# Kernel optimization log

Hardware: AMD Instinct MI355X
Metric: run time of the kernel (lower is better)

The kernel has to match this reference:

```python
import jax, jax.numpy as jnp
import numpy as np

ALPHA_MIN = float(np.exp(-1.0 / 5.0))   # 0.8187
ALPHA_MAX = float(np.exp(-1.0 / 25.0))  # 0.9608
THRESHOLD = 1.0


def setup_inputs() -> dict:
    key = jax.random.key(0)
    k_x, k_w, k_a, k_u, k_s = jax.random.split(key, 5)
    B, T, I, H = 64, 1000, 1024, 1024
    x = jax.random.normal(k_x, (B, T, I), dtype=jnp.float32)
    # nn.Linear default init ~ U(-1/sqrt(I), 1/sqrt(I)); gaussian of similar scale is fine
    W = jax.random.normal(k_w, (H, I), dtype=jnp.float32) / np.sqrt(I)
    alpha = jax.random.uniform(k_a, (H,), dtype=jnp.float32,
                               minval=ALPHA_MIN, maxval=ALPHA_MAX)
    # original uses torch.rand for initial membrane potential / spikes
    u0 = jax.random.uniform(k_u, (B, H), dtype=jnp.float32)
    s0 = jax.random.uniform(k_s, (B, H), dtype=jnp.float32)
    return {"x": x, "W": W, "alpha": alpha, "u0": u0, "s0": s0}


def reference(x, W, alpha, u0, s0):
    # Input projection: Wx[b,t,h] = sum_i x[b,t,i] * W[h,i]
    Wx = jnp.einsum('bti,hi->bth', x, W)
    a = jnp.clip(alpha, ALPHA_MIN, ALPHA_MAX)  # [H]

    def step(carry, wx_t):
        ut, st = carry                              # each [B, H]
        ut = a * (ut - st) + (1.0 - a) * wx_t       # leaky integrate with reset
        st = (ut - THRESHOLD > 0).astype(ut.dtype)  # hard spike (boxcar surrogate in bwd)
        return (ut, st), st

    # scan over time: Wx -> [T, B, H]
    _, s = jax.lax.scan(step, (u0, s0), jnp.swapaxes(Wx, 0, 1))
    return jnp.swapaxes(s, 0, 1)  # [B, T, H]
```

## Files before the change

kernel.cpp:

```cpp
#include <hip/hip_runtime.h>


#define TM 128
#define TN 64
#define TK 8
#define LDA 130

__global__ __launch_bounds__(256) void transpose_w(
    const float* __restrict__ W, double* __restrict__ WdT)
{
    __shared__ float t[32][33];
    const int k0 = blockIdx.x * 32;
    const int n0 = blockIdx.y * 32;
    const int tx = threadIdx.x & 31;
    const int ty = threadIdx.x >> 5;
    #pragma unroll
    for (int i = 0; i < 4; i++)
        t[ty + 8 * i][tx] = W[(size_t)(n0 + ty + 8 * i) * 1024 + k0 + tx];
    __syncthreads();
    #pragma unroll
    for (int i = 0; i < 4; i++)
        WdT[(size_t)(k0 + ty + 8 * i) * 1024 + n0 + tx] = (double)t[tx][ty + 8 * i];
}

__global__ __launch_bounds__(256, 3) void gemm_f64_sgpr(
    const float* __restrict__ A,
    const double* __restrict__ WdT,
    double* __restrict__ C, int M, int N, int K)
{
    __shared__ double As[2][TK][LDA];

    const int tid  = threadIdx.x;
    const int lane = tid & 63;
    const int nb = __builtin_amdgcn_readfirstlane(blockIdx.x * TN + (tid >> 6) * 16);
    const int tm = blockIdx.y * TM;

    const int kq = (tid & 1) * 4;
    const int r  = tid >> 1;

    double acc0[16], acc1[16];
    #pragma unroll
    for (int j = 0; j < 16; j++) { acc0[j] = 0.0; acc1[j] = 0.0; }

    const int ar = min(tm + r, M - 1);
    const float* Ap = A + (size_t)ar * K + kq;

    {
        const float4 a0 = *(const float4*)(Ap);
        As[0][kq + 0][r] = (double)a0.x; As[0][kq + 1][r] = (double)a0.y;
        As[0][kq + 2][r] = (double)a0.z; As[0][kq + 3][r] = (double)a0.w;
    }
    __syncthreads();

    auto compute_tile = [&](int p, int k0) {
        #pragma unroll
        for (int kk = 0; kk < TK; kk++) {
            const double* wr = WdT + (size_t)(k0 + kk) * N + nb;
            const double2 a = *(const double2*)&As[p][kk][2 * lane];
            #pragma unroll
            for (int j = 0; j < 16; j++) {
                const double wj = wr[j];
                acc0[j] = fma(a.x, wj, acc0[j]);
                acc1[j] = fma(a.y, wj, acc1[j]);
            }
        }
    };

    const int NS = K / TK;
    for (int s = 0; s < NS - 1; ++s) {
        const int p = s & 1;
        {
            const float4 a0 = *(const float4*)(Ap + (size_t)(s + 1) * TK);
            const int q = 1 - p;
            As[q][kq + 0][r] = (double)a0.x; As[q][kq + 1][r] = (double)a0.y;
            As[q][kq + 2][r] = (double)a0.z; As[q][kq + 3][r] = (double)a0.w;
        }
        compute_tile(p, s * TK);
        __syncthreads();
    }
    compute_tile((NS - 1) & 1, (NS - 1) * TK);

    const int m0 = tm + 2 * lane;
    if (m0 < M) {
        double* Cr = C + (size_t)m0 * N + nb;
        #pragma unroll
        for (int j = 0; j < 8; j++)
            *(double2*)&Cr[2 * j] = double2{acc0[2 * j], acc0[2 * j + 1]};
    }
    if (m0 + 1 < M) {
        double* Cr = C + (size_t)(m0 + 1) * N + nb;
        #pragma unroll
        for (int j = 0; j < 8; j++)
            *(double2*)&Cr[2 * j] = double2{acc1[2 * j], acc1[2 * j + 1]};
    }
}

__global__ __launch_bounds__(256) void lif_scan_kernel(
    const double* __restrict__ Wx,
    const float* __restrict__ alpha,
    const float* __restrict__ u0,
    const float* __restrict__ s0,
    float* __restrict__ out,
    int b0, int T, int H)
{
    const int idx = blockIdx.x * blockDim.x + threadIdx.x;
    const int h  = idx & 1023;
    const int bl = idx >> 10;
    const int b  = b0 + bl;

    const double AMIN = 0.8187307530779818;
    const double AMAX = 0.9607894391523232;
    double a = (double)alpha[h];
    a = fmin(fmax(a, AMIN), AMAX);
    const double oma = 1.0 - a;

    double u = (double)u0[(size_t)b * H + h];
    double s = (double)s0[(size_t)b * H + h];

    const double* wp = Wx + (size_t)bl * T * H + h;
    float* op = out + (size_t)b * T * H + h;

    double v[8];
    #pragma unroll
    for (int p = 0; p < 8; p++) v[p] = wp[(size_t)p * H];

    for (int t0 = 0; t0 < T; t0 += 8) {
        double nv[8];
        const bool more = (t0 + 8) < T;
        const double* wn = wp + (size_t)(t0 + 8) * H;
        #pragma unroll
        for (int p = 0; p < 8; p++) nv[p] = more ? wn[(size_t)p * H] : 0.0;

        #pragma unroll
        for (int p = 0; p < 8; p++) {
            u = a * (u - s) + oma * v[p];
            s = (u - 1.0 > 0.0) ? 1.0 : 0.0;
            op[(size_t)(t0 + p) * H] = (float)s;
        }
        #pragma unroll
        for (int p = 0; p < 8; p++) v[p] = nv[p];
    }
}

extern "C" void kernel_launch(void* const* d_in, const int* in_sizes, int n_in,
                              void* d_out, int out_size, void* d_ws, size_t ws_size,
                              hipStream_t stream) {
    const float* x     = (const float*)d_in[0];
    const float* W     = (const float*)d_in[1];
    const float* alpha = (const float*)d_in[2];
    const float* u0    = (const float*)d_in[3];
    const float* s0    = (const float*)d_in[4];
    float* out = (float*)d_out;
    const int Bt = 64, T = 1000, I = 1024, H = 1024;

    double* wdT = (double*)d_ws;
    const size_t wdT_bytes = (size_t)I * H * sizeof(double);
    double* wx = (double*)((char*)d_ws + wdT_bytes);
    const size_t avail = (ws_size > wdT_bytes) ? ws_size - wdT_bytes : 0;

    const size_t per_batch = (size_t)T * H * sizeof(double);
    int Bc = 1;
    {
        const int cands[7] = {64, 32, 16, 8, 4, 2, 1};
        for (int c = 0; c < 7; c++) {
            if ((size_t)cands[c] * per_batch <= avail) { Bc = cands[c]; break; }
        }
    }

    transpose_w<<<dim3(1024 / 32, 1024 / 32), 256, 0, stream>>>(W, wdT);

    for (int b0 = 0; b0 < Bt; b0 += Bc) {
        const int M = Bc * T;
        dim3 grid(H / TN, (M + TM - 1) / TM);
        gemm_f64_sgpr<<<grid, 256, 0, stream>>>(
            x + (size_t)b0 * T * I, wdT, wx, M, H, I);
        lif_scan_kernel<<<(Bc * H) / 256, 256, 0, stream>>>(
            wx, alpha, u0, s0, out, b0, T, H);
    }
}
```

Before: 2.989 ms.

## Use FP64 MFMA matrix cores for input projection GEMM with runtime layout probe

Adds an FP64 GEMM built on the 16x16x4 f64 MFMA instruction, with both A and W tiles staged in shared memory and double-buffered. A one-wavefront probe kernel works out the MFMA operand and result layout at runtime and stores it in a flag. The MFMA kernel reads that flag and the old scalar FMA kernel serves as a fallback, so both are launched every batch chunk and one exits early. The goal is to move the dominant FP64 GEMM off the vector ALUs onto the matrix cores, at the cost of an extra kernel launch per chunk and a small probe kernel.

After: 2.438 ms. 1.23x faster.

```diff
diff --git a/kernel.cpp b/kernel.cpp
--- a/kernel.cpp
+++ b/kernel.cpp
@@ -3,8 +3,12 @@
 
 #define TM 128
 #define TN 64
-#define TK 8
+#define MTK 16
+#define VTK 8
 #define LDA 130
+#define LDB 66
+
+typedef double v4d __attribute__((ext_vector_type(4)));
 
 __global__ __launch_bounds__(256) void transpose_w(
     const float* __restrict__ W, double* __restrict__ WdT)
@@ -23,12 +27,180 @@
         WdT[(size_t)(k0 + ty + 8 * i) * 1024 + n0 + tx] = (double)t[tx][ty + 8 * i];
 }
 
+__global__ __launch_bounds__(64) void probe_mfma_layout(unsigned int* __restrict__ flag)
+{
+    __shared__ double Am[16][4];
+    __shared__ double Bm[4][16];
+    const int l = threadIdx.x;
+    Am[l & 15][l >> 4] = (double)(1 + (l & 15) + 16 * (l >> 4));
+    Bm[l >> 4][l & 15] = 1.0 + 0.5 * (double)((l >> 4) + 4 * (l & 15));
+    __syncthreads();
+    const v4d z = {0.0, 0.0, 0.0, 0.0};
+    const double a0 = Am[l & 15][l >> 4];
+    const double b0 = Bm[l >> 4][l & 15];
+    const double a1 = Am[l >> 2][l & 3];
+    const double b1 = Bm[l & 3][l >> 2];
+    const v4d d0 = __builtin_amdgcn_mfma_f64_16x16x4f64(a0, b0, z, 0, 0, 0);
+    const v4d d1 = __builtin_amdgcn_mfma_f64_16x16x4f64(a1, b1, z, 0, 0, 0);
+    int ok[8];
+    #pragma unroll
+    for (int c = 0; c < 8; c++) ok[c] = 1;
+    #pragma unroll
+    for (int q = 0; q < 4; q++) {
+        const int iD[4] = {4 * (l >> 4) + q, l & 15, (l >> 4) + 4 * q, l & 15};
+        const int jD[4] = {l & 15, 4 * (l >> 4) + q, l & 15, (l >> 4) + 4 * q};
+        #pragma unroll
+        for (int dm = 0; dm < 4; dm++) {
+            double ref = 0.0;
+            #pragma unroll
+            for (int k = 0; k < 4; k++) ref += Am[iD[dm]][k] * Bm[k][jD[dm]];
+            if (d0[q] != ref) ok[dm] = 0;
+            if (d1[q] != ref) ok[4 + dm] = 0;
+        }
+    }
+    unsigned int f = 255u;
+    for (int c = 7; c >= 0; --c)
+        if (__all(ok[c])) f = (unsigned int)c;
+    if (l == 0) *flag = f;
+}
+
+__global__ __launch_bounds__(256, 3) void gemm_f64_mfma(
+    const float* __restrict__ A,
+    const double* __restrict__ WdT,
+    double* __restrict__ C, int M, int N, int K,
+    const unsigned int* __restrict__ flag)
+{
+    const unsigned int f = *flag;
+    if (f - 1u > 6u) return;
+
+    __shared__ double As[2][MTK][LDA];
+    __shared__ double Bs[2][MTK][LDB];
+
+    const int tid  = threadIdx.x;
+    const int lane = tid & 63;
+    const int l16  = lane & 15;
+    const int kq4  = lane >> 4;
+    const int wid  = tid >> 6;
+    const int wr   = wid >> 1;
+    const int wc   = wid & 1;
+
+    const int imap = (int)(f >> 2);
+    const int dmap = (int)(f & 3u);
+    const int rowl = imap ? (lane >> 2) : l16;
+    const int kl   = imap ? (lane & 3)  : kq4;
+    int rloc, rstep, cloc, cstep;
+    switch (dmap) {
+        case 0:  rloc = 4 * kq4; rstep = 1; cloc = l16;     cstep = 0; break;
+        case 1:  rloc = l16;     rstep = 0; cloc = 4 * kq4; cstep = 1; break;
+        case 2:  rloc = kq4;     rstep = 4; cloc = l16;     cstep = 0; break;
+        default: rloc = l16;     rstep = 0; cloc = kq4;     cstep = 4; break;
+    }
+
+    const int nb0 = blockIdx.x * TN;
+    const int tm  = blockIdx.y * TM;
+
+    const int rA  = tid >> 1;
+    const int kA  = (tid & 1) * 4;
+    const int kkB = tid >> 4;
+    const int cBl = (tid & 15) * 4;
+
+    v4d acc[4][2];
+    #pragma unroll
+    for (int i = 0; i < 4; i++)
+        #pragma unroll
+        for (int j = 0; j < 2; j++)
+            acc[i][j] = (v4d)0.0;
+
+    const int ar = min(tm + rA, M - 1);
+    const float* Apg = A + (size_t)ar * K;
+    const double* Bpg = WdT + (size_t)kkB * N + nb0 + cBl;
+
+    struct StReg { float4 a0, a1; double2 b0, b1; };
+    auto issue = [&](int s) {
+        StReg t;
+        const int k0 = s * MTK;
+        t.a0 = *(const float4*)(Apg + k0 + kA);
+        t.a1 = *(const float4*)(Apg + k0 + kA + 8);
+        const double* wp = Bpg + (size_t)k0 * N;
+        t.b0 = *(const double2*)(wp);
+        t.b1 = *(const double2*)(wp + 2);
+        return t;
+    };
+    auto commit = [&](int buf, const StReg& t) {
+        As[buf][kA + 0][rA] = (double)t.a0.x;
+        As[buf][kA + 1][rA] = (double)t.a0.y;
+        As[buf][kA + 2][rA] = (double)t.a0.z;
+        As[buf][kA + 3][rA] = (double)t.a0.w;
+        As[buf][kA + 8][rA] = (double)t.a1.x;
+        As[buf][kA + 9][rA] = (double)t.a1.y;
+        As[buf][kA + 10][rA] = (double)t.a1.z;
+        As[buf][kA + 11][rA] = (double)t.a1.w;
+        Bs[buf][kkB][cBl + 0] = t.b0.x;
+        Bs[buf][kkB][cBl + 1] = t.b0.y;
+        Bs[buf][kkB][cBl + 2] = t.b1.x;
+        Bs[buf][kkB][cBl + 3] = t.b1.y;
+    };
+
+    const int mw = wr * 64;
+    const int nw = wc * 32;
+    auto compute_tile = [&](int p) {
+        #pragma unroll
+        for (int ks = 0; ks < 4; ++ks) {
+            const int kk = ks * 4 + kl;
+            double av[4], bv[2];
+            #pragma unroll
+            for (int i = 0; i < 4; i++) av[i] = As[p][kk][mw + i * 16 + rowl];
+            #pragma unroll
+            for (int j = 0; j < 2; j++) bv[j] = Bs[p][kk][nw + j * 16 + rowl];
+            #pragma unroll
+            for (int i = 0; i < 4; i++)
+                #pragma unroll
+                for (int j = 0; j < 2; j++)
+                    acc[i][j] = __builtin_amdgcn_mfma_f64_16x16x4f64(
+                        av[i], bv[j], acc[i][j], 0, 0, 0);
+        }
+    };
+
+    commit(0, issue(0));
+    __syncthreads();
+
+    const int NR = K / MTK;
+    for (int s = 0; s < NR - 1; ++s) {
+        const int p = s & 1;
+        StReg t = issue(s + 1);
+        compute_tile(p);
+        commit(1 - p, t);
+        __syncthreads();
+    }
+    compute_tile((NR - 1) & 1);
+
+    const int mwR = tm + mw;
+    const int nwC = nb0 + nw;
+    #pragma unroll
+    for (int i = 0; i < 4; i++) {
+        #pragma unroll
+        for (int q = 0; q < 4; q++) {
+            const int row = mwR + i * 16 + rloc + q * rstep;
+            if (row < M) {
+                double* Cr = C + (size_t)row * N + nwC + cloc + q * cstep;
+                Cr[0]  = acc[i][0][q];
+                Cr[16] = acc[i][1][q];
+            }
+        }
+    }
+}
+
 __global__ __launch_bounds__(256, 3) void gemm_f64_sgpr(
     const float* __restrict__ A,
     const double* __restrict__ WdT,
-    double* __restrict__ C, int M, int N, int K)
-{
-    __shared__ double As[2][TK][LDA];
+    double* __restrict__ C, int M, int N, int K,
+    const unsigned int* __restrict__ flag)
+{
+    {
+        const unsigned int f = *flag;
+        if (f - 1u <= 6u) return;
+    }
+    __shared__ double As[2][VTK][LDA];
 
     const int tid  = threadIdx.x;
     const int lane = tid & 63;
@@ -54,7 +226,7 @@
 
     auto compute_tile = [&](int p, int k0) {
         #pragma unroll
-        for (int kk = 0; kk < TK; kk++) {
+        for (int kk = 0; kk < VTK; kk++) {
             const double* wr = WdT + (size_t)(k0 + kk) * N + nb;
             const double2 a = *(const double2*)&As[p][kk][2 * lane];
             #pragma unroll
@@ -66,19 +238,19 @@
         }
     };
 
-    const int NS = K / TK;
+    const int NS = K / VTK;
     for (int s = 0; s < NS - 1; ++s) {
         const int p = s & 1;
         {
-            const float4 a0 = *(const float4*)(Ap + (size_t)(s + 1) * TK);
+            const float4 a0 = *(const float4*)(Ap + (size_t)(s + 1) * VTK);
             const int q = 1 - p;
             As[q][kq + 0][r] = (double)a0.x; As[q][kq + 1][r] = (double)a0.y;
             As[q][kq + 2][r] = (double)a0.z; As[q][kq + 3][r] = (double)a0.w;
         }
-        compute_tile(p, s * TK);
+        compute_tile(p, s * VTK);
         __syncthreads();
     }
-    compute_tile((NS - 1) & 1, (NS - 1) * TK);
+    compute_tile((NS - 1) & 1, (NS - 1) * VTK);
 
     const int m0 = tm + 2 * lane;
     if (m0 < M) {
@@ -155,8 +327,10 @@
 
     double* wdT = (double*)d_ws;
     const size_t wdT_bytes = (size_t)I * H * sizeof(double);
+    const size_t flag_off = (ws_size - 256) & ~(size_t)255;
+    unsigned int* flag = (unsigned int*)((char*)d_ws + flag_off);
     double* wx = (double*)((char*)d_ws + wdT_bytes);
-    const size_t avail = (ws_size > wdT_bytes) ? ws_size - wdT_bytes : 0;
+    const size_t avail = (flag_off > wdT_bytes) ? flag_off - wdT_bytes : 0;
 
     const size_t per_batch = (size_t)T * H * sizeof(double);
     int Bc = 1;
@@ -168,12 +342,15 @@
     }
 
     transpose_w<<<dim3(1024 / 32, 1024 / 32), 256, 0, stream>>>(W, wdT);
+    probe_mfma_layout<<<1, 64, 0, stream>>>(flag);
 
     for (int b0 = 0; b0 < Bt; b0 += Bc) {
         const int M = Bc * T;
         dim3 grid(H / TN, (M + TM - 1) / TM);
+        gemm_f64_mfma<<<grid, 256, 0, stream>>>(
+            x + (size_t)b0 * T * I, wdT, wx, M, H, I, flag);
         gemm_f64_sgpr<<<grid, 256, 0, stream>>>(
-            x + (size_t)b0 * T * I, wdT, wx, M, H, I);
+            x + (size_t)b0 * T * I, wdT, wx, M, H, I, flag);
         lif_scan_kernel<<<(Bc * H) / 256, 256, 0, stream>>>(
             wx, alpha, u0, s0, out, b0, T, H);
     }
```
